# Optimization experiments

Measured on AMD Instinct MI355X. Metric: run time of the kernel, lower is better.

## Reference

```python
import jax, jax.numpy as jnp
import numpy as np

DECAY = 0.6
GAIN = 0.4


def _layernorm(x, g, b, eps=1e-5):
    m = x.mean(-1, keepdims=True)
    v = x.var(-1, keepdims=True)
    return (x - m) * jax.lax.rsqrt(v + eps) * g + b


def _ema_scan(x, axis, reverse=False):
    # linear recurrence state = 0.6*state + 0.4*x as an associative scan
    a = jnp.full_like(x, DECAY)
    b = GAIN * x
    def comb(c1, c2):
        a1, b1 = c1
        a2, b2 = c2
        return a1 * a2, a2 * b1 + b2
    _, y = jax.lax.associative_scan(comb, (a, b), axis=axis, reverse=reverse)
    return y


def setup_inputs() -> dict:
    key = jax.random.key(0)
    B, H, W, D = 16, 64, 64, 384
    inner = 2 * D
    hidden = 4 * D
    ks = jax.random.split(key, 12)
    s = 0.02
    return {
        "x": jax.random.normal(ks[0], (B, H, W, D), jnp.float32),
        "n1_g": jnp.ones((D,), jnp.float32),
        "n1_b": jnp.zeros((D,), jnp.float32),
        "w_in": s * jax.random.normal(ks[1], (D, inner), jnp.float32),
        "b_in": jnp.zeros((inner,), jnp.float32),
        "k_conv": s * jax.random.normal(ks[2], (3, 3, 1, inner), jnp.float32),  # depthwise HWIO
        "on_g": jnp.ones((inner,), jnp.float32),
        "on_b": jnp.zeros((inner,), jnp.float32),
        "w_out": s * jax.random.normal(ks[3], (inner, D), jnp.float32),
        "b_out": jnp.zeros((D,), jnp.float32),
        "n2_g": jnp.ones((D,), jnp.float32),
        "n2_b": jnp.zeros((D,), jnp.float32),
        "w1": s * jax.random.normal(ks[4], (D, hidden), jnp.float32),
        "b1": jnp.zeros((hidden,), jnp.float32),
        "w2": s * jax.random.normal(ks[5], (hidden, D), jnp.float32),
        "b2": jnp.zeros((D,), jnp.float32),
    }


def reference(x, n1_g, n1_b, w_in, b_in, k_conv, on_g, on_b, w_out, b_out,
              n2_g, n2_b, w1, b1, w2, b2):
    inner = w_in.shape[1]
    # --- LegacyScan2DOperator branch ---
    h = _layernorm(x, n1_g, n1_b)
    p = h @ w_in + b_in  # [B,H,W,inner]
    local = jax.lax.conv_general_dilated(
        p, k_conv, window_strides=(1, 1), padding="SAME",
        dimension_numbers=("NHWC", "HWIO", "NHWC"),
        feature_group_count=inner)
    lr = _ema_scan(local, axis=2)                 # left->right over W
    rl = _ema_scan(local, axis=2, reverse=True)   # right->left
    tb = _ema_scan(local, axis=1)                 # top->bottom over H
    bt = _ema_scan(local, axis=1, reverse=True)   # bottom->top
    mixed = 0.25 * (lr + rl + tb + bt) + local
    mixed = _layernorm(mixed, on_g, on_b)
    x = x + (mixed @ w_out + b_out)
    # --- MLP branch ---
    h2 = _layernorm(x, n2_g, n2_b)
    m = jax.nn.gelu(h2 @ w1 + b1, approximate=False) @ w2 + b2
    return x + m
```

## Files before the change

### kernel.cpp

```cpp
#include <hip/hip_runtime.h>
#include <math.h>


typedef __attribute__((ext_vector_type(8))) short bf16x8;
typedef __attribute__((ext_vector_type(4))) float f32x4;

#define T_TOKENS 65536
#define DMODEL 384
#define DINNER 768
#define DHIDDEN 1536

__device__ __forceinline__ float bf2f(unsigned short u) {
  unsigned int x = ((unsigned int)u) << 16;
  return __builtin_bit_cast(float, x);
}
__device__ __forceinline__ unsigned short f2bf(float f) {
  unsigned int x = __builtin_bit_cast(unsigned int, f);
  x += 0x7fffu + ((x >> 16) & 1u);
  return (unsigned short)(x >> 16);
}
__device__ __forceinline__ void unpack2(unsigned int u, float& lo, float& hi) {
  lo = __builtin_bit_cast(float, u << 16);
  hi = __builtin_bit_cast(float, u & 0xffff0000u);
}
__device__ __forceinline__ unsigned int pack2(float lo, float hi) {
  return (unsigned int)f2bf(lo) | ((unsigned int)f2bf(hi) << 16);
}
__device__ __forceinline__ unsigned int pack2t(float lo, float hi) {
  return (__builtin_bit_cast(unsigned int, lo) >> 16) |
         (__builtin_bit_cast(unsigned int, hi) & 0xffff0000u);
}

__device__ __forceinline__ void gload16(const void* g, void* l) {
  __builtin_amdgcn_global_load_lds(
      (const __attribute__((address_space(1))) void*)g,
      (__attribute__((address_space(3))) void*)l, 16, 0, 0);
}

__global__ __launch_bounds__(256) void ln_fused_f32_384(
    const float* __restrict__ in, const float* __restrict__ g,
    const float* __restrict__ b, unsigned short* __restrict__ out) {
  const int tok = blockIdx.x * 4 + (threadIdx.x >> 6);
  const int lane = threadIdx.x & 63;
  const float2* row = (const float2*)(in + (size_t)tok * 384);
  float2 v[3];
  float s = 0.f, ss = 0.f;
#pragma unroll
  for (int k = 0; k < 3; k++) {
    v[k] = row[lane + 64 * k];
    s += v[k].x + v[k].y;
    ss += v[k].x * v[k].x + v[k].y * v[k].y;
  }
#pragma unroll
  for (int off = 32; off > 0; off >>= 1) {
    s += __shfl_xor(s, off);
    ss += __shfl_xor(ss, off);
  }
  const float m = s * (1.0f / 384.0f);
  const float r = rsqrtf(ss * (1.0f / 384.0f) - m * m + 1e-5f);
  unsigned int* op = (unsigned int*)(out + (size_t)tok * 384);
#pragma unroll
  for (int k = 0; k < 3; k++) {
    const int c = lane + 64 * k;
    const float2 gg = ((const float2*)g)[c];
    const float2 bb = ((const float2*)b)[c];
    op[c] = pack2((v[k].x - m) * r * gg.x + bb.x, (v[k].y - m) * r * gg.y + bb.y);
  }
}

__global__ __launch_bounds__(256) void ln_bundle_768(
    const uint2* __restrict__ mixed, const float* __restrict__ g,
    const float* __restrict__ b, uint2* __restrict__ out) {
  const int tid = threadIdx.x;
  const int tk = tid >> 2, j = tid & 3;
  const int token = blockIdx.x * 64 + tk;
  const int bb_ = token >> 12, posb = token & 4095;
  const size_t slab = (size_t)bb_ * 4096 + posb;
  float s = 0.f, ss = 0.f;
#pragma unroll 1
  for (int cg = j; cg < 192; cg += 4) {
    const uint2 v = mixed[((size_t)cg * 16) * 4096 + slab];
    float e0, e1, e2, e3;
    unpack2(v.x, e0, e1);
    unpack2(v.y, e2, e3);
    s += (e0 + e1) + (e2 + e3);
    ss += e0 * e0 + e1 * e1 + e2 * e2 + e3 * e3;
  }
  s += __shfl_xor(s, 1); ss += __shfl_xor(ss, 1);
  s += __shfl_xor(s, 2); ss += __shfl_xor(ss, 2);
  const float m = s * (1.0f / 768.0f);
  const float r = rsqrtf(ss * (1.0f / 768.0f) - m * m + 1e-5f);
  const size_t tokbase = (size_t)token * 192;
#pragma unroll 1
  for (int cg = j; cg < 192; cg += 4) {
    const uint2 v = mixed[((size_t)cg * 16) * 4096 + slab];
    const float4 gg = ((const float4*)g)[cg];
    const float4 bb4 = ((const float4*)b)[cg];
    float e0, e1, e2, e3;
    unpack2(v.x, e0, e1);
    unpack2(v.y, e2, e3);
    uint2 o;
    o.x = pack2((e0 - m) * r * gg.x + bb4.x, (e1 - m) * r * gg.y + bb4.y);
    o.y = pack2((e2 - m) * r * gg.z + bb4.z, (e3 - m) * r * gg.w + bb4.w);
    out[tokbase + cg] = o;
  }
}

__global__ __launch_bounds__(256) void wprep_kernel(const float* __restrict__ in,
                                                    unsigned short* __restrict__ out,
                                                    int K, int N) {
  __shared__ float t[32][33];
  const int k0 = blockIdx.x * 32, n0 = blockIdx.y * 32;
  const int a = threadIdx.x & 31, b8 = threadIdx.x >> 5;
#pragma unroll
  for (int i = 0; i < 4; i++)
    t[b8 + 8 * i][a] = in[(size_t)(k0 + b8 + 8 * i) * N + n0 + a];
  __syncthreads();
#pragma unroll
  for (int i = 0; i < 4; i++)
    out[(size_t)(n0 + b8 + 8 * i) * K + k0 + a] = f2bf(t[a][b8 + 8 * i]);
}

template <int EPI>
__global__ __launch_bounds__(256) void gemm_bt_kernel(
    const unsigned short* __restrict__ A, int lda,
    const unsigned short* __restrict__ Bt, int ldb, int KT,
    const float* __restrict__ bias, const float* __restrict__ res,
    void* __restrict__ C, int ldc, int nby) {
  __shared__ unsigned short smem[32768];
  char* const smc = (char*)smem;

  const int tid = threadIdx.x;
  const int w = tid >> 6, lane = tid & 63;
  const int cpx = gridDim.x >> 3;
  const int g = blockIdx.x;
  const int sw = (g & 7) * cpx + (g >> 3);
  const int bx = sw / nby, by = sw - bx * nby;
  const int tok0 = bx << 7, n0 = by << 7;

  const int wm = w >> 1, wn = w & 1;
  const int lrow = lane & 15, kgrp = lane >> 4;
  const int cx = lrow & 7;

  const int lr8 = lane >> 3;
  const int kce = ((lane & 7) ^ lr8) << 3;
  const unsigned short* Abase = A + (size_t)(tok0 + w * 32 + lr8) * lda + kce;
  const unsigned short* Bbase = Bt + (size_t)(n0 + w * 32 + lr8) * ldb + kce;

  f32x4 acc[4][4];
#pragma unroll
  for (int i = 0; i < 4; i++)
#pragma unroll
    for (int j = 0; j < 4; j++) {
      f32x4 z = {0.f, 0.f, 0.f, 0.f};
      acc[i][j] = z;
    }

  const int nt = KT >> 6;
#pragma unroll
  for (int i = 0; i < 4; i++) {
    gload16(Abase + (size_t)i * 8 * lda, smc + (w * 4 + i) * 1024);
    gload16(Bbase + (size_t)i * 8 * ldb, smc + 32768 + (w * 4 + i) * 1024);
  }
  __syncthreads();

  int buf = 0;
  for (int t = 0; t < nt; t++) {
    if (t + 1 < nt) {
      const int kt = (t + 1) << 6;
      const int bo = (buf ^ 1) * 16384;
#pragma unroll
      for (int i = 0; i < 4; i++) {
        gload16(Abase + (size_t)i * 8 * lda + kt, smc + bo + (w * 4 + i) * 1024);
        gload16(Bbase + (size_t)i * 8 * ldb + kt,
                smc + 32768 + bo + (w * 4 + i) * 1024);
      }
    }
    bf16x8 af[2][4], bf_[2][4];
    const int bo = buf * 16384;
#pragma unroll
    for (int ks = 0; ks < 2; ks++) {
#pragma unroll
      for (int f = 0; f < 4; f++) {
        const int co = ((ks * 4 + kgrp) ^ cx) << 4;
        af[ks][f] =
            *(const bf16x8*)(smc + bo + (wm * 64 + f * 16 + lrow) * 128 + co);
        bf_[ks][f] = *(const bf16x8*)(smc + 32768 + bo +
                                      (wn * 64 + f * 16 + lrow) * 128 + co);
      }
    }
#pragma unroll
    for (int ks = 0; ks < 2; ks++)
#pragma unroll
      for (int mf = 0; mf < 4; mf++)
#pragma unroll
        for (int nf = 0; nf < 4; nf++)
          acc[mf][nf] = __builtin_amdgcn_mfma_f32_16x16x32_bf16(
              af[ks][mf], bf_[ks][nf], acc[mf][nf], 0, 0, 0);
    __syncthreads();
    buf ^= 1;
  }

  if constexpr (EPI == 3) {
#pragma unroll
    for (int mf = 0; mf < 4; mf++)
#pragma unroll
      for (int nf = 0; nf < 4; nf++) {
        const int cl = wn * 64 + nf * 16 + lrow;
        const float bv = bias[n0 + cl];
#pragma unroll
        for (int r = 0; r < 4; r++) {
          const int tl = wm * 64 + mf * 16 + kgrp * 4 + r;
          smem[(cl >> 2) * 520 + tl * 4 + (cl & 3)] =
              f2bf(acc[mf][nf][r] + bv);
        }
      }
    __syncthreads();
    const int bb_ = tok0 >> 12, pos0 = tok0 & 4095, cg0 = n0 >> 2;
    uint2* Cb = (uint2*)C;
#pragma unroll
    for (int e = 0; e < 16; e++) {
      const int lin = e * 256 + tid;
      const int cgl = lin >> 7, pp = lin & 127;
      const uint2 v = *(const uint2*)&smem[cgl * 520 + pp * 4];
      Cb[((size_t)(cg0 + cgl) * 16 + bb_) * 4096 + pos0 + pp] = v;
    }
  } else {
#pragma unroll
    for (int mf = 0; mf < 4; mf++) {
#pragma unroll
      for (int nf = 0; nf < 4; nf++) {
        const int gcol = n0 + wn * 64 + nf * 16 + lrow;
        const float bv = bias ? bias[gcol] : 0.0f;
#pragma unroll
        for (int r = 0; r < 4; r++) {
          const int grow = tok0 + wm * 64 + mf * 16 + kgrp * 4 + r;
          float v = acc[mf][nf][r] + bv;
          const size_t idx = (size_t)grow * ldc + gcol;
          if constexpr (EPI == 1) {
            ((float*)C)[idx] = v + res[idx];
          } else {
            const float z = 1.5957691216057308f * (v + 0.044715f * v * v * v);
            const float gl = v / (1.0f + __expf(-z));
            ((unsigned short*)C)[idx] = f2bf(gl);
          }
        }
      }
    }
  }
}

__device__ __forceinline__ void ema_seg_f(const unsigned int vals[16],
                                          const int seg, float rl[16],
                                          float rh[16]) {
  const float A16 = 2.8211099e-4f;
  const float A32 = 7.9586611e-8f;
  float a, bv, t;
  float za = 0.f, zb = 0.f;
#pragma unroll
  for (int j = 0; j < 16; j++) {
    unpack2(vals[j], a, bv);
    za = 0.6f * za + 0.4f * a;
    zb = 0.6f * zb + 0.4f * bv;
  }
  t = __shfl_up(za, 1); if (seg >= 1) za += A16 * t;
  t = __shfl_up(zb, 1); if (seg >= 1) zb += A16 * t;
  t = __shfl_up(za, 2); if (seg >= 2) za += A32 * t;
  t = __shfl_up(zb, 2); if (seg >= 2) zb += A32 * t;
  float yfa = __shfl_up(za, 1), yfb = __shfl_up(zb, 1);
  if (seg == 0) { yfa = 0.f; yfb = 0.f; }
  float ua = 0.f, ub = 0.f;
#pragma unroll
  for (int j = 15; j >= 0; j--) {
    unpack2(vals[j], a, bv);
    ua = 0.6f * ua + 0.4f * a;
    ub = 0.6f * ub + 0.4f * bv;
  }
  t = __shfl_down(ua, 1); if (seg <= 2) ua += A16 * t;
  t = __shfl_down(ub, 1); if (seg <= 2) ub += A16 * t;
  t = __shfl_down(ua, 2); if (seg <= 1) ua += A32 * t;
  t = __shfl_down(ub, 2); if (seg <= 1) ub += A32 * t;
  float zba = __shfl_down(ua, 1), zbb = __shfl_down(ub, 1);
  if (seg == 3) { zba = 0.f; zbb = 0.f; }
  float fa = yfa, fb = yfb;
#pragma unroll
  for (int j = 0; j < 16; j++) {
    unpack2(vals[j], a, bv);
    fa = 0.6f * fa + 0.4f * a;
    fb = 0.6f * fb + 0.4f * bv;
    rl[j] = fa;
    rh[j] = fb;
  }
  float ga = zba, gb = zbb;
#pragma unroll
  for (int j = 15; j >= 0; j--) {
    unpack2(vals[j], a, bv);
    ga = 0.6f * ga + 0.4f * a;
    gb = 0.6f * gb + 0.4f * bv;
    rl[j] = 0.25f * (rl[j] + ga);
    rh[j] = 0.25f * (rh[j] + gb);
  }
}

__global__ __launch_bounds__(512) void conv_scan_kernel(
    const uint2* __restrict__ p, const float* __restrict__ kconv,
    uint2* __restrict__ mixed) {
  __shared__ unsigned int loc[2][64][65];
  __shared__ float klds[36];
  const int tid = threadIdx.x;
  const int c = blockIdx.x;
  const int b = blockIdx.y;
  const uint2* pb = p + ((size_t)c * 16 + b) * 4096;

  if (tid < 36) klds[tid] = kconv[(tid >> 2) * DINNER + c * 4 + (tid & 3)];
  __syncthreads();

#pragma unroll 1
  for (int i = 0; i < 8; i++) {
    const int pos = tid + 512 * i;
    const int h = pos >> 6, w = pos & 63;
    float a0 = 0.f, a1 = 0.f, a2 = 0.f, a3 = 0.f;
#pragma unroll
    for (int dh = 0; dh < 3; dh++) {
      const int hh = h + dh - 1;
      const bool vh = (unsigned)hh < 64u;
      const int hcl = min(max(hh, 0), 63);
#pragma unroll
      for (int dw = 0; dw < 3; dw++) {
        const int ww = w + dw - 1;
        const bool vv = vh && ((unsigned)ww < 64u);
        const int wcl = min(max(ww, 0), 63);
        uint2 pv = pb[hcl * 64 + wcl];
        if (!vv) { pv.x = 0; pv.y = 0; }
        const int t = dh * 3 + dw;
        float lo, hi;
        unpack2(pv.x, lo, hi);
        a0 += lo * klds[t * 4 + 0];
        a1 += hi * klds[t * 4 + 1];
        unpack2(pv.y, lo, hi);
        a2 += lo * klds[t * 4 + 2];
        a3 += hi * klds[t * 4 + 3];
      }
    }
    loc[0][h][w] = pack2t(a0, a1);
    loc[1][h][w] = pack2t(a2, a3);
  }
  __syncthreads();

  const int seg = tid & 3;
  const int ax = (tid >> 2) & 63;
  const int cp = tid >> 8;
  const int j0 = seg * 16;

  float hcl_[16], hch_[16];
  {
    unsigned int vals[16];
#pragma unroll
    for (int j = 0; j < 16; j++) vals[j] = loc[cp][j0 + j][ax];
    ema_seg_f(vals, seg, hcl_, hch_);
  }
  __syncthreads();

  {
    unsigned int vals[16];
    float wl[16], wh[16];
#pragma unroll
    for (int j = 0; j < 16; j++) vals[j] = loc[cp][ax][j0 + j];
    ema_seg_f(vals, seg, wl, wh);
#pragma unroll
    for (int j = 0; j < 16; j++) {
      float a, bv;
      unpack2(vals[j], a, bv);
      loc[cp][ax][j0 + j] = pack2t(a + wl[j], bv + wh[j]);
    }
  }
  __syncthreads();

#pragma unroll
  for (int j = 0; j < 16; j++) {
    float a, bv;
    unpack2(loc[cp][j0 + j][ax], a, bv);
    loc[cp][j0 + j][ax] = pack2t(a + hcl_[j], bv + hch_[j]);
  }
  __syncthreads();

  uint2* mb = mixed + ((size_t)c * 16 + b) * 4096;
#pragma unroll 1
  for (int i = 0; i < 8; i++) {
    const int pos = tid + 512 * i;
    const int h = pos >> 6, w = pos & 63;
    uint2 st;
    st.x = loc[0][h][w];
    st.y = loc[1][h][w];
    mb[pos] = st;
  }
}

extern "C" void kernel_launch(void* const* d_in, const int* in_sizes, int n_in,
                              void* d_out, int out_size, void* d_ws,
                              size_t ws_size, hipStream_t stream) {
  const float* x = (const float*)d_in[0];
  const float* n1_g = (const float*)d_in[1];
  const float* n1_b = (const float*)d_in[2];
  const float* w_in = (const float*)d_in[3];
  const float* b_in = (const float*)d_in[4];
  const float* k_conv = (const float*)d_in[5];
  const float* on_g = (const float*)d_in[6];
  const float* on_b = (const float*)d_in[7];
  const float* w_out = (const float*)d_in[8];
  const float* b_out = (const float*)d_in[9];
  const float* n2_g = (const float*)d_in[10];
  const float* n2_b = (const float*)d_in[11];
  const float* w1 = (const float*)d_in[12];
  const float* b1 = (const float*)d_in[13];
  const float* w2 = (const float*)d_in[14];
  const float* b2 = (const float*)d_in[15];

  const size_t MB = 1024 * 1024;
  char* ws = (char*)d_ws;
  unsigned short* R1 = (unsigned short*)(ws + 3 * MB / 2);
  unsigned short* R2 = (unsigned short*)(ws + 3 * MB / 2 + 96 * MB);

  unsigned short* A1 = R2;
  unsigned short* wTin = R2 + (48 * MB) / 2;
  unsigned short* p = R1;
  unsigned short* A2 = R2;
  unsigned short* wTout = R1;
  unsigned short* A3 = R1;
  unsigned short* wT1 = R1 + (48 * MB) / 2;
  unsigned short* wT2 = wT1 + (size_t)1536 * 384;
  unsigned short* gb = R2;

  float* out = (float*)d_out;
  dim3 b256(256);

  ln_fused_f32_384<<<T_TOKENS / 4, b256, 0, stream>>>(x, n1_g, n1_b, A1);
  wprep_kernel<<<dim3(12, 24), b256, 0, stream>>>(w_in, wTin, DMODEL, DINNER);
  gemm_bt_kernel<3><<<3072, b256, 0, stream>>>(A1, DMODEL, wTin, DMODEL, DMODEL,
                                               b_in, nullptr, p, DINNER, 6);
  conv_scan_kernel<<<dim3(192, 16), dim3(512), 0, stream>>>(
      (const uint2*)p, k_conv, (uint2*)p);
  ln_bundle_768<<<1024, b256, 0, stream>>>((const uint2*)p, on_g, on_b,
                                           (uint2*)A2);
  wprep_kernel<<<dim3(24, 12), b256, 0, stream>>>(w_out, wTout, DINNER, DMODEL);
  gemm_bt_kernel<1><<<1536, b256, 0, stream>>>(A2, DINNER, wTout, DINNER, DINNER,
                                               b_out, x, out, DMODEL, 3);
  ln_fused_f32_384<<<T_TOKENS / 4, b256, 0, stream>>>(out, n2_g, n2_b, A3);
  wprep_kernel<<<dim3(12, 48), b256, 0, stream>>>(w1, wT1, DMODEL, DHIDDEN);
  wprep_kernel<<<dim3(48, 12), b256, 0, stream>>>(w2, wT2, DHIDDEN, DMODEL);
  for (int hh = 0; hh < 2; hh++) {
    const size_t toff = (size_t)hh * 32768;
    gemm_bt_kernel<2><<<3072, b256, 0, stream>>>(
        A3 + toff * DMODEL, DMODEL, wT1, DMODEL, DMODEL, b1, nullptr, gb,
        DHIDDEN, 12);
    gemm_bt_kernel<1><<<768, b256, 0, stream>>>(
        gb, DHIDDEN, wT2, DHIDDEN, DHIDDEN, b2, out + toff * DMODEL,
        out + toff * DMODEL, DMODEL, 3);
  }
}
```

Baseline: 677.6 us.

## Halve GEMM K-tile to 32 and shrink LDS for higher occupancy

The bf16 GEMM kernel now stages 32-wide K slices instead of 64, which halves shared memory per block. It also adds a launch bound of 4 blocks per CU so more blocks can be resident to hide memory latency. In exchange there are twice as many loop iterations and barriers per K, fewer MFMAs per sync, and a new XOR swizzle for the 64-byte rows that could raise LDS bank conflicts. The epilogue reuses smem, so the smaller buffer must still fit its staging layout.

After: 663.6 us. -2.1%, faster.

```diff
diff --git a/kernel.cpp b/kernel.cpp
--- a/kernel.cpp
+++ b/kernel.cpp
@@ -122,12 +122,12 @@
 }
 
 template <int EPI>
-__global__ __launch_bounds__(256) void gemm_bt_kernel(
+__global__ __launch_bounds__(256, 4) void gemm_bt_kernel(
     const unsigned short* __restrict__ A, int lda,
     const unsigned short* __restrict__ Bt, int ldb, int KT,
     const float* __restrict__ bias, const float* __restrict__ res,
     void* __restrict__ C, int ldc, int nby) {
-  __shared__ unsigned short smem[32768];
+  __shared__ unsigned short smem[16640];
   char* const smc = (char*)smem;
 
   const int tid = threadIdx.x;
@@ -140,12 +140,18 @@
 
   const int wm = w >> 1, wn = w & 1;
   const int lrow = lane & 15, kgrp = lane >> 4;
-  const int cx = lrow & 7;
-
-  const int lr8 = lane >> 3;
-  const int kce = ((lane & 7) ^ lr8) << 3;
-  const unsigned short* Abase = A + (size_t)(tok0 + w * 32 + lr8) * lda + kce;
-  const unsigned short* Bbase = Bt + (size_t)(n0 + w * 32 + lr8) * ldb + kce;
+
+  const int lr4 = lane >> 2;
+  const int r0 = (w * 2 + 0) * 16 + lr4;
+  const int r1 = (w * 2 + 1) * 16 + lr4;
+  const int c0 = ((lane & 3) ^ ((r0 >> 1) & 3)) << 3;
+  const int c1 = ((lane & 3) ^ ((r1 >> 1) & 3)) << 3;
+  const unsigned short* A0 = A + (size_t)(tok0 + r0) * lda + c0;
+  const unsigned short* A1p = A + (size_t)(tok0 + r1) * lda + c1;
+  const unsigned short* B0 = Bt + (size_t)(n0 + r0) * ldb + c0;
+  const unsigned short* B1 = Bt + (size_t)(n0 + r1) * ldb + c1;
+  const int d0 = (w * 2 + 0) * 1024;
+  const int d1 = (w * 2 + 1) * 1024;
 
   f32x4 acc[4][4];
 #pragma unroll
@@ -156,47 +162,40 @@
       acc[i][j] = z;
     }
 
-  const int nt = KT >> 6;
-#pragma unroll
-  for (int i = 0; i < 4; i++) {
-    gload16(Abase + (size_t)i * 8 * lda, smc + (w * 4 + i) * 1024);
-    gload16(Bbase + (size_t)i * 8 * ldb, smc + 32768 + (w * 4 + i) * 1024);
-  }
+  const int nt = KT >> 5;
+  gload16(A0, smc + d0);
+  gload16(A1p, smc + d1);
+  gload16(B0, smc + 16384 + d0);
+  gload16(B1, smc + 16384 + d1);
   __syncthreads();
 
   int buf = 0;
   for (int t = 0; t < nt; t++) {
     if (t + 1 < nt) {
-      const int kt = (t + 1) << 6;
-      const int bo = (buf ^ 1) * 16384;
-#pragma unroll
-      for (int i = 0; i < 4; i++) {
-        gload16(Abase + (size_t)i * 8 * lda + kt, smc + bo + (w * 4 + i) * 1024);
-        gload16(Bbase + (size_t)i * 8 * ldb + kt,
-                smc + 32768 + bo + (w * 4 + i) * 1024);
-      }
-    }
-    bf16x8 af[2][4], bf_[2][4];
-    const int bo = buf * 16384;
-#pragma unroll
-    for (int ks = 0; ks < 2; ks++) {
-#pragma unroll
-      for (int f = 0; f < 4; f++) {
-        const int co = ((ks * 4 + kgrp) ^ cx) << 4;
-        af[ks][f] =
-            *(const bf16x8*)(smc + bo + (wm * 64 + f * 16 + lrow) * 128 + co);
-        bf_[ks][f] = *(const bf16x8*)(smc + 32768 + bo +
-                                      (wn * 64 + f * 16 + lrow) * 128 + co);
-      }
-    }
-#pragma unroll
-    for (int ks = 0; ks < 2; ks++)
-#pragma unroll
-      for (int mf = 0; mf < 4; mf++)
-#pragma unroll
-        for (int nf = 0; nf < 4; nf++)
-          acc[mf][nf] = __builtin_amdgcn_mfma_f32_16x16x32_bf16(
-              af[ks][mf], bf_[ks][nf], acc[mf][nf], 0, 0, 0);
+      const int kt = (t + 1) << 5;
+      const int bo = (buf ^ 1) * 8192;
+      gload16(A0 + kt, smc + bo + d0);
+      gload16(A1p + kt, smc + bo + d1);
+      gload16(B0 + kt, smc + 16384 + bo + d0);
+      gload16(B1 + kt, smc + 16384 + bo + d1);
+    }
+    const int bo = buf * 8192;
+    bf16x8 af[4], bf_[4];
+#pragma unroll
+    for (int f = 0; f < 4; f++) {
+      const int ra = wm * 64 + f * 16 + lrow;
+      const int rb = wn * 64 + f * 16 + lrow;
+      af[f] = *(const bf16x8*)(smc + bo + ra * 64 +
+                               ((kgrp ^ ((ra >> 1) & 3)) << 4));
+      bf_[f] = *(const bf16x8*)(smc + 16384 + bo + rb * 64 +
+                                ((kgrp ^ ((rb >> 1) & 3)) << 4));
+    }
+#pragma unroll
+    for (int mf = 0; mf < 4; mf++)
+#pragma unroll
+      for (int nf = 0; nf < 4; nf++)
+        acc[mf][nf] = __builtin_amdgcn_mfma_f32_16x16x32_bf16(
+            af[mf], bf_[nf], acc[mf][nf], 0, 0, 0);
     __syncthreads();
     buf ^= 1;
   }
```
